# Optimization experiments

Measured on AMD Instinct MI355X. Metric: run time of the kernel, lower is better.

Reference implementation:

```python
import jax, jax.numpy as jnp
import numpy as np
import math

B, T, C, H = 4, 1024, 1024, 16
D = C // H  # head dim = 64

def setup_inputs() -> dict:
    key = jax.random.key(0)
    ks = jax.random.split(key, 10)
    s = 1.0 / math.sqrt(C)
    x = jax.random.normal(ks[0], (B, T, C), dtype=jnp.float32)
    pad = (jax.random.uniform(ks[1], (B, T)) < 0.2).astype(jnp.float32)
    # ensure first token of every row is unpadded so softmax rows are well-posed
    pad = pad.at[:, 0].set(0.0)
    Wq = jax.random.normal(ks[2], (C, C), dtype=jnp.float32) * s
    bq = jnp.zeros((C,), dtype=jnp.float32)
    Wk = jax.random.normal(ks[3], (C, C), dtype=jnp.float32) * s
    bk = jnp.zeros((C,), dtype=jnp.float32)
    Wv = jax.random.normal(ks[4], (C, C), dtype=jnp.float32) * s
    bv = jnp.zeros((C,), dtype=jnp.float32)
    Wp = jax.random.normal(ks[5], (C, C), dtype=jnp.float32) * s
    bp = jnp.zeros((C,), dtype=jnp.float32)
    return {"x": x, "x_padding_judge": pad, "Wq": Wq, "bq": bq,
            "Wk": Wk, "bk": bk, "Wv": Wv, "bv": bv, "Wp": Wp, "bp": bp}

def reference(x, x_padding_judge, Wq, bq, Wk, bk, Wv, bv, Wp, bp):
    # keep flag: 1.0 where token is real, 0.0 where padded
    keep = 1.0 - x_padding_judge                      # [B, T]
    mask = keep[:, :, None] * keep[:, None, :]        # [B, T, T] outer product
    # projections, split heads: [B, H, T, D]
    def heads(w, b):
        return (x @ w + b).reshape(B, T, H, D).transpose(0, 2, 1, 3)
    q, k, v = heads(Wq, bq), heads(Wk, bk), heads(Wv, bv)
    att = jnp.einsum('bhqd,bhkd->bhqk', q, k) * (1.0 / math.sqrt(D))
    # attn_pdrop=0 => att_full is all ones; masked_fill where mask == 0
    att = jnp.where(mask[:, None, :, :] == 0, -1e9, att)
    att = jax.nn.softmax(att, axis=-1)
    y = jnp.einsum('bhqk,bhkd->bhqd', att, v)         # [B, H, T, D]
    y = y.transpose(0, 2, 1, 3).reshape(B, T, C)
    return y @ Wp + bp
```

## Files before the change

kernel.cpp:

```cpp
#include <hip/hip_runtime.h>
#include <hip/hip_bf16.h>
#include <math.h>

#define Bb 4
#define Tt 1024
#define Cc 1024
#define Hh 16
#define Dd 64

typedef __attribute__((ext_vector_type(8))) _Float16 half8;
typedef __attribute__((ext_vector_type(4))) _Float16 half4;
typedef __attribute__((ext_vector_type(4))) float floatx4;

__device__ __forceinline__ void gl2lds16(const void* g, void* l) {
    __builtin_amdgcn_global_load_lds(
        (const __attribute__((address_space(1))) void*)g,
        (__attribute__((address_space(3))) void*)l,
        16, 0, 0);
}

__global__ __launch_bounds__(256) void convert_fp16(const float* __restrict__ s,
                                                    _Float16* __restrict__ d)
{
    const size_t i = ((size_t)blockIdx.x * 256 + threadIdx.x) * 8;
    float4 a = *(const float4*)(s + i);
    float4 b = *(const float4*)(s + i + 4);
    half8 h;
    h[0] = (_Float16)a.x; h[1] = (_Float16)a.y; h[2] = (_Float16)a.z; h[3] = (_Float16)a.w;
    h[4] = (_Float16)b.x; h[5] = (_Float16)b.y; h[6] = (_Float16)b.z; h[7] = (_Float16)b.w;
    *(half8*)(d + i) = h;
}

struct WPrep { const float* W[4]; _Float16* out[4]; };

__global__ __launch_bounds__(256) void prep_weights(WPrep p)
{
    const int z = blockIdx.z;
    const float* __restrict__ W = p.W[z];
    _Float16* __restrict__ outp = p.out[z];
    __shared__ float tile[64][65];
    const int k0  = blockIdx.y * 64;
    const int n0  = blockIdx.x * 64;
    const int tr  = threadIdx.x >> 4;
    const int tc4 = (threadIdx.x & 15) * 4;

#pragma unroll
    for (int i = 0; i < 4; ++i) {
        const int kk = tr + i * 16;
        float4 v = *(const float4*)(W + (size_t)(k0 + kk) * 1024 + n0 + tc4);
        tile[kk][tc4 + 0] = v.x;
        tile[kk][tc4 + 1] = v.y;
        tile[kk][tc4 + 2] = v.z;
        tile[kk][tc4 + 3] = v.w;
    }
    __syncthreads();
#pragma unroll
    for (int i = 0; i < 4; ++i) {
        const int n = tr + i * 16;
        half4 h;
#pragma unroll
        for (int c = 0; c < 4; ++c) h[c] = (_Float16)tile[tc4 + c][n];
        *(half4*)(outp + (size_t)(n0 + n) * 1024 + k0 + tc4) = h;
    }
}

struct QkvP { const _Float16* Wt[3]; const float* bias[3];
              _Float16* qb; _Float16* kb; _Float16* vt; };

__global__ __launch_bounds__(256) void gemm_qkv(const _Float16* __restrict__ xh, QkvP p)
{
    const int z = blockIdx.z;
    const _Float16* __restrict__ Wt   = p.Wt[z];
    const float* __restrict__    bias = p.bias[z];

    __shared__ __align__(16) _Float16 As[2][4096];
    __shared__ __align__(16) _Float16 Bs[2][4096];

    const int tid  = threadIdx.x;
    const int lane = tid & 63;
    const int w    = tid >> 6;
    const int wr   = w >> 1, wc = w & 1;
    const int quad = lane >> 4;
    const int l15  = lane & 15;
    const int bm   = blockIdx.x * 128;
    const int bn   = blockIdx.y * 128;

    const int c0 = tid, c1 = tid + 256;
    const _Float16* Ag0 = xh + (size_t)(bm + (c0 & 127)) * 1024 + (c0 >> 7) * 8;
    const _Float16* Ag1 = xh + (size_t)(bm + (c1 & 127)) * 1024 + (c1 >> 7) * 8;
    const _Float16* Bg0 = Wt + (size_t)(bn + (c0 & 127)) * 1024 + (c0 >> 7) * 8;
    const _Float16* Bg1 = Wt + (size_t)(bn + (c1 & 127)) * 1024 + (c1 >> 7) * 8;

    floatx4 acc[4][4];
#pragma unroll
    for (int i = 0; i < 4; ++i)
#pragma unroll
        for (int j = 0; j < 4; ++j)
            acc[i][j] = (floatx4){0.f, 0.f, 0.f, 0.f};

    half8 sA0 = *(const half8*)(Ag0);
    half8 sA1 = *(const half8*)(Ag1);
    half8 sB0 = *(const half8*)(Bg0);
    half8 sB1 = *(const half8*)(Bg1);
    *(half8*)&As[0][c0 * 8] = sA0;
    *(half8*)&As[0][c1 * 8] = sA1;
    *(half8*)&Bs[0][c0 * 8] = sB0;
    *(half8*)&Bs[0][c1 * 8] = sB1;
    sA0 = *(const half8*)(Ag0 + 32);
    sA1 = *(const half8*)(Ag1 + 32);
    sB0 = *(const half8*)(Bg0 + 32);
    sB1 = *(const half8*)(Bg1 + 32);
    __syncthreads();

#pragma unroll 2
    for (int kt = 0; kt < 1024; kt += 32) {
        const int cur = (kt >> 5) & 1;
        const int nxt = cur ^ 1;
        const int kf = (kt + 64 < 1024) ? kt + 64 : kt;
        half8 fA0 = *(const half8*)(Ag0 + kf);
        half8 fA1 = *(const half8*)(Ag1 + kf);
        half8 fB0 = *(const half8*)(Bg0 + kf);
        half8 fB1 = *(const half8*)(Bg1 + kf);

        half8 a[4], b[4];
#pragma unroll
        for (int i = 0; i < 4; ++i)
            a[i] = *(const half8*)&As[cur][(quad * 128 + wr * 64 + i * 16 + l15) * 8];
#pragma unroll
        for (int j = 0; j < 4; ++j)
            b[j] = *(const half8*)&Bs[cur][(quad * 128 + wc * 64 + j * 16 + l15) * 8];
#pragma unroll
        for (int i = 0; i < 4; ++i)
#pragma unroll
            for (int j = 0; j < 4; ++j)
                acc[i][j] = __builtin_amdgcn_mfma_f32_16x16x32_f16(a[i], b[j], acc[i][j], 0, 0, 0);

        *(half8*)&As[nxt][c0 * 8] = sA0;
        *(half8*)&As[nxt][c1 * 8] = sA1;
        *(half8*)&Bs[nxt][c0 * 8] = sB0;
        *(half8*)&Bs[nxt][c1 * 8] = sB1;
        __syncthreads();
        sA0 = fA0; sA1 = fA1; sB0 = fB0; sB1 = fB1;
    }

    if (z == 2) {
#pragma unroll
        for (int j = 0; j < 4; ++j) {
            const int col = bn + wc * 64 + j * 16 + l15;
            const int h = col >> 6, dd = col & 63;
            const float bj = bias[col];
#pragma unroll
            for (int i = 0; i < 4; ++i) {
                const int t0 = bm + wr * 64 + i * 16 + quad * 4;
                const int bi = t0 >> 10, t = t0 & 1023;
                half4 pk;
#pragma unroll
                for (int r = 0; r < 4; ++r) pk[r] = (_Float16)(acc[i][j][r] + bj);
                *(half4*)(p.vt + ((size_t)(bi * 16 + h) * 64 + dd) * 1024 + t) = pk;
            }
        }
    } else {
        _Float16* outp = (z == 0) ? p.qb : p.kb;
#pragma unroll
        for (int j = 0; j < 4; ++j) {
            const int col = bn + wc * 64 + j * 16 + l15;
            const int h = col >> 6, dd = col & 63;
            const float bj = bias[col];
#pragma unroll
            for (int i = 0; i < 4; ++i) {
#pragma unroll
                for (int r = 0; r < 4; ++r) {
                    const int tg = bm + wr * 64 + i * 16 + quad * 4 + r;
                    const int bi = tg >> 10, t = tg & 1023;
                    outp[((size_t)(bi * 16 + h) * 1024 + t) * 64 + dd] =
                        (_Float16)(acc[i][j][r] + bj);
                }
            }
        }
    }
}

__global__ __launch_bounds__(256) void attn_mfma(
    const _Float16* __restrict__ qb, const _Float16* __restrict__ kb,
    const _Float16* __restrict__ vt, const float* __restrict__ padj,
    _Float16* __restrict__ yh)
{
    __shared__ __align__(16) _Float16 Qs[8192];
    __shared__ __align__(16) _Float16 Ks[4096];
    __shared__ __align__(16) _Float16 Vt[4096];
    __shared__ __align__(16) _Float16 Ps[8192];
    __shared__ float keepq_s[128];
    __shared__ float keepk_s[64];

    const int tid  = threadIdx.x;
    const int lane = tid & 63;
    const int w    = tid >> 6;
    const int quad = lane >> 4;
    const int l15  = lane & 15;
    const int bh   = blockIdx.x;
    const int q0   = blockIdx.y * 128;
    const int b    = bh >> 4;
    const int h    = bh & 15;

    const _Float16* qbase = qb + (size_t)bh * Tt * Dd;
    const _Float16* kbase = kb + (size_t)bh * Tt * Dd;
    const _Float16* vbase = vt + (size_t)bh * Dd * Tt;

#pragma unroll
    for (int it = 0; it < 4; ++it) {
        const int c = it * 256 + tid;
        const int row = c & 127, kc = c >> 7;
        gl2lds16(qbase + (size_t)(q0 + row) * 64 + kc * 8, Qs + (c >> 6) * 512);
    }
    if (tid < 128) keepq_s[tid] = 1.0f - padj[b * Tt + q0 + tid];

    floatx4 O[2][4];
    floatx4 l_acc[2];
#pragma unroll
    for (int mi = 0; mi < 2; ++mi) {
#pragma unroll
        for (int dj = 0; dj < 4; ++dj) O[mi][dj] = (floatx4){0.f, 0.f, 0.f, 0.f};
        l_acc[mi] = (floatx4){0.f, 0.f, 0.f, 0.f};
    }

    half8 ones;
#pragma unroll
    for (int j = 0; j < 8; ++j) ones[j] = (_Float16)1.0f;

    constexpr float SC = 0.18033688011112042f;

    for (int kt = 0; kt < Tt; kt += 64) {
        __syncthreads();

#pragma unroll
        for (int it = 0; it < 2; ++it) {
            const int c = it * 256 + tid;
            const int key = c & 63, kc = c >> 6;
            gl2lds16(kbase + (size_t)(kt + key) * 64 + kc * 8, Ks + (c >> 6) * 512);
        }
#pragma unroll
        for (int it = 0; it < 2; ++it) {
            const int c = it * 256 + tid;
            const int dd = c & 63, kc = c >> 6;
            gl2lds16(vbase + (size_t)dd * 1024 + kt + kc * 8, Vt + (c >> 6) * 512);
        }
        if (tid < 64) keepk_s[tid] = 1.0f - padj[b * Tt + kt + tid];
        __syncthreads();

        floatx4 ST[4][2];
#pragma unroll
        for (int mk = 0; mk < 4; ++mk)
#pragma unroll
            for (int nq = 0; nq < 2; ++nq)
                ST[mk][nq] = (floatx4){0.f, 0.f, 0.f, 0.f};
#pragma unroll
        for (int ks = 0; ks < 2; ++ks) {
            half8 ak[4], bq[2];
#pragma unroll
            for (int mk = 0; mk < 4; ++mk)
                ak[mk] = *(const half8*)&Ks[((ks * 4 + quad) * 64 + mk * 16 + l15) * 8];
#pragma unroll
            for (int nq = 0; nq < 2; ++nq)
                bq[nq] = *(const half8*)&Qs[((ks * 4 + quad) * 128 + w * 32 + nq * 16 + l15) * 8];
#pragma unroll
            for (int mk = 0; mk < 4; ++mk)
#pragma unroll
                for (int nq = 0; nq < 2; ++nq)
                    ST[mk][nq] = __builtin_amdgcn_mfma_f32_16x16x32_f16(ak[mk], bq[nq], ST[mk][nq], 0, 0, 0);
        }

        const float kq0 = keepq_s[w * 32 + l15];
        const float kq1 = keepq_s[w * 32 + 16 + l15];
#pragma unroll
        for (int mk = 0; mk < 4; ++mk) {
            const float4 kk4 = *(const float4*)&keepk_s[mk * 16 + quad * 4];
            const float kkr[4] = {kk4.x, kk4.y, kk4.z, kk4.w};
#pragma unroll
            for (int nq = 0; nq < 2; ++nq) {
                const float kq = nq ? kq1 : kq0;
                half4 pk;
#pragma unroll
                for (int r = 0; r < 4; ++r) {
                    const float e = __builtin_amdgcn_exp2f(ST[mk][nq][r] * SC);
                    const float p = (kq == 0.0f) ? 1.0f : kkr[r] * e;
                    pk[r] = (_Float16)p;
                }
                *(half4*)&Ps[((mk * 2 + (quad >> 1)) * 128 + w * 32 + nq * 16 + l15) * 8 + (quad & 1) * 4] = pk;
            }
        }
        __syncthreads();

#pragma unroll
        for (int ks = 0; ks < 2; ++ks) {
            half8 ap[2], bv[4];
#pragma unroll
            for (int mi = 0; mi < 2; ++mi)
                ap[mi] = *(const half8*)&Ps[((ks * 4 + quad) * 128 + w * 32 + mi * 16 + l15) * 8];
#pragma unroll
            for (int dj = 0; dj < 4; ++dj)
                bv[dj] = *(const half8*)&Vt[((ks * 4 + quad) * 64 + dj * 16 + l15) * 8];
#pragma unroll
            for (int mi = 0; mi < 2; ++mi) {
#pragma unroll
                for (int dj = 0; dj < 4; ++dj)
                    O[mi][dj] = __builtin_amdgcn_mfma_f32_16x16x32_f16(ap[mi], bv[dj], O[mi][dj], 0, 0, 0);
                l_acc[mi] = __builtin_amdgcn_mfma_f32_16x16x32_f16(ap[mi], ones, l_acc[mi], 0, 0, 0);
            }
        }
    }

#pragma unroll
    for (int mi = 0; mi < 2; ++mi) {
#pragma unroll
        for (int r = 0; r < 4; ++r) {
            const int rowl = w * 32 + mi * 16 + quad * 4 + r;
            const int token = b * Tt + q0 + rowl;
            const float inv = 1.0f / l_acc[mi][r];
#pragma unroll
            for (int dj = 0; dj < 4; ++dj) {
                const int col = h * 64 + dj * 16 + l15;
                yh[(size_t)token * 1024 + col] = (_Float16)(O[mi][dj][r] * inv);
            }
        }
    }
}

__global__ __launch_bounds__(256) void gemm_proj(const _Float16* __restrict__ Ay,
                                                 const _Float16* __restrict__ Bt,
                                                 const float* __restrict__ bias,
                                                 float* __restrict__ out)
{
    __shared__ __align__(16) _Float16 As[2][4096];
    __shared__ __align__(16) _Float16 Bs[2][2048];

    const int tid  = threadIdx.x;
    const int lane = tid & 63;
    const int w    = tid >> 6;
    const int quad = lane >> 4;
    const int l15  = lane & 15;
    const int bm   = blockIdx.x * 128;
    const int bn   = blockIdx.y * 64;

    const int c0 = tid, c1 = tid + 256;
    const _Float16* Ag0 = Ay + (size_t)(bm + (c0 & 127)) * 1024 + (c0 >> 7) * 8;
    const _Float16* Ag1 = Ay + (size_t)(bm + (c1 & 127)) * 1024 + (c1 >> 7) * 8;
    const _Float16* Bg0 = Bt + (size_t)(bn + (c0 & 63)) * 1024 + (c0 >> 6) * 8;

    floatx4 acc[2][4];
#pragma unroll
    for (int i = 0; i < 2; ++i)
#pragma unroll
        for (int j = 0; j < 4; ++j)
            acc[i][j] = (floatx4){0.f, 0.f, 0.f, 0.f};

    half8 sA0 = *(const half8*)(Ag0);
    half8 sA1 = *(const half8*)(Ag1);
    half8 sB0 = *(const half8*)(Bg0);
    *(half8*)&As[0][c0 * 8] = sA0;
    *(half8*)&As[0][c1 * 8] = sA1;
    *(half8*)&Bs[0][c0 * 8] = sB0;
    sA0 = *(const half8*)(Ag0 + 32);
    sA1 = *(const half8*)(Ag1 + 32);
    sB0 = *(const half8*)(Bg0 + 32);
    __syncthreads();

#pragma unroll 2
    for (int kt = 0; kt < 1024; kt += 32) {
        const int cur = (kt >> 5) & 1;
        const int nxt = cur ^ 1;
        const int kf = (kt + 64 < 1024) ? kt + 64 : kt;
        half8 fA0 = *(const half8*)(Ag0 + kf);
        half8 fA1 = *(const half8*)(Ag1 + kf);
        half8 fB0 = *(const half8*)(Bg0 + kf);

        half8 a[2], b[4];
#pragma unroll
        for (int i = 0; i < 2; ++i)
            a[i] = *(const half8*)&As[cur][(quad * 128 + w * 32 + i * 16 + l15) * 8];
#pragma unroll
        for (int j = 0; j < 4; ++j)
            b[j] = *(const half8*)&Bs[cur][(quad * 64 + j * 16 + l15) * 8];
#pragma unroll
        for (int i = 0; i < 2; ++i)
#pragma unroll
            for (int j = 0; j < 4; ++j)
                acc[i][j] = __builtin_amdgcn_mfma_f32_16x16x32_f16(a[i], b[j], acc[i][j], 0, 0, 0);

        *(half8*)&As[nxt][c0 * 8] = sA0;
        *(half8*)&As[nxt][c1 * 8] = sA1;
        *(half8*)&Bs[nxt][c0 * 8] = sB0;
        __syncthreads();
        sA0 = fA0; sA1 = fA1; sB0 = fB0;
    }

#pragma unroll
    for (int j = 0; j < 4; ++j) {
        const int col = bn + j * 16 + l15;
        const float bj = bias[col];
#pragma unroll
        for (int i = 0; i < 2; ++i) {
            const int row = bm + w * 32 + i * 16 + quad * 4;
            float* o = out + (size_t)row * 1024 + col;
#pragma unroll
            for (int r = 0; r < 4; ++r)
                o[(size_t)r * 1024] = acc[i][j][r] + bj;
        }
    }
}

extern "C" void kernel_launch(void* const* d_in, const int* in_sizes, int n_in,
                              void* d_out, int out_size, void* d_ws, size_t ws_size,
                              hipStream_t stream)
{
    const float* x    = (const float*)d_in[0];
    const float* padj = (const float*)d_in[1];
    const float* Wq   = (const float*)d_in[2];
    const float* bq   = (const float*)d_in[3];
    const float* Wk   = (const float*)d_in[4];
    const float* bk   = (const float*)d_in[5];
    const float* Wv   = (const float*)d_in[6];
    const float* bv   = (const float*)d_in[7];
    const float* Wp   = (const float*)d_in[8];
    const float* bp   = (const float*)d_in[9];
    float* out = (float*)d_out;

    const size_t MB = 1024 * 1024;
    char* ws = (char*)d_ws;
    _Float16* xh  = (_Float16*)(ws);
    _Float16* Wt0 = (_Float16*)(ws +  8 * MB);
    _Float16* Wt1 = (_Float16*)(ws + 10 * MB);
    _Float16* Wt2 = (_Float16*)(ws + 12 * MB);
    _Float16* Wtp = (_Float16*)(ws + 14 * MB);
    _Float16* qb  = (_Float16*)(ws + 16 * MB);
    _Float16* kb  = (_Float16*)(ws + 24 * MB);
    _Float16* vtb = (_Float16*)(ws + 32 * MB);
    _Float16* yh  = (_Float16*)(ws + 40 * MB);

    convert_fp16<<<2048, 256, 0, stream>>>(x, xh);

    WPrep wp;
    wp.W[0] = Wq; wp.W[1] = Wk; wp.W[2] = Wv; wp.W[3] = Wp;
    wp.out[0] = Wt0; wp.out[1] = Wt1; wp.out[2] = Wt2; wp.out[3] = Wtp;
    prep_weights<<<dim3(16, 16, 4), 256, 0, stream>>>(wp);

    QkvP qp;
    qp.Wt[0] = Wt0; qp.Wt[1] = Wt1; qp.Wt[2] = Wt2;
    qp.bias[0] = bq; qp.bias[1] = bk; qp.bias[2] = bv;
    qp.qb = qb; qp.kb = kb; qp.vt = vtb;
    gemm_qkv<<<dim3(32, 8, 3), 256, 0, stream>>>(xh, qp);

    attn_mfma<<<dim3(64, 8), 256, 0, stream>>>(qb, kb, vtb, padj, yh);

    gemm_proj<<<dim3(32, 16), 256, 0, stream>>>(yh, Wtp, bp, out);
}
```

Baseline: 213.6 us.

## Pre-swizzle operands into MFMA fragment layout and drop LDS staging in GEMMs

The fp16 copies of x, the weights and the attention output are now written in a tiled layout in which each 16-row by 32-k MFMA fragment is a contiguous 1 KB block. This lets the QKV and projection GEMMs load operand fragments straight from global memory into registers with no LDS staging and no __syncthreads. The cost is that operand reuse across waves now relies on L2/L1 caching instead of shared memory, so global traffic per block goes up. The reworked convert kernel also launches 256 blocks, each converting a 16-row strip.

```diff
diff --git a/kernel.cpp b/kernel.cpp
--- a/kernel.cpp
+++ b/kernel.cpp
@@ -12,6 +12,7 @@
 typedef __attribute__((ext_vector_type(4))) _Float16 half4;
 typedef __attribute__((ext_vector_type(4))) float floatx4;
 
+
 __device__ __forceinline__ void gl2lds16(const void* g, void* l) {
     __builtin_amdgcn_global_load_lds(
         (const __attribute__((address_space(1))) void*)g,
@@ -22,13 +23,21 @@
 __global__ __launch_bounds__(256) void convert_fp16(const float* __restrict__ s,
                                                     _Float16* __restrict__ d)
 {
-    const size_t i = ((size_t)blockIdx.x * 256 + threadIdx.x) * 8;
-    float4 a = *(const float4*)(s + i);
-    float4 b = *(const float4*)(s + i + 4);
-    half8 h;
-    h[0] = (_Float16)a.x; h[1] = (_Float16)a.y; h[2] = (_Float16)a.z; h[3] = (_Float16)a.w;
-    h[4] = (_Float16)b.x; h[5] = (_Float16)b.y; h[6] = (_Float16)b.z; h[7] = (_Float16)b.w;
-    *(half8*)(d + i) = h;
+    const int m16 = blockIdx.x;
+    const int r   = threadIdx.x & 15;
+    const int kc0 = threadIdx.x >> 4;
+    const float* src = s + (size_t)(m16 * 16 + r) * 1024;
+    _Float16*   dst = d + (size_t)m16 * 16384 + r * 8;
+#pragma unroll
+    for (int c8 = 0; c8 < 8; ++c8) {
+        const int kc = kc0 + c8 * 16;
+        float4 a = *(const float4*)(src + kc * 8);
+        float4 b = *(const float4*)(src + kc * 8 + 4);
+        half8 h;
+        h[0] = (_Float16)a.x; h[1] = (_Float16)a.y; h[2] = (_Float16)a.z; h[3] = (_Float16)a.w;
+        h[4] = (_Float16)b.x; h[5] = (_Float16)b.y; h[6] = (_Float16)b.z; h[7] = (_Float16)b.w;
+        *(half8*)(dst + kc * 128) = h;
+    }
 }
 
 struct WPrep { const float* W[4]; _Float16* out[4]; };
@@ -56,11 +65,12 @@
     __syncthreads();
 #pragma unroll
     for (int i = 0; i < 4; ++i) {
-        const int n = tr + i * 16;
         half4 h;
 #pragma unroll
-        for (int c = 0; c < 4; ++c) h[c] = (_Float16)tile[tc4 + c][n];
-        *(half4*)(outp + (size_t)(n0 + n) * 1024 + k0 + tc4) = h;
+        for (int c = 0; c < 4; ++c) h[c] = (_Float16)tile[tc4 + c][tr + i * 16];
+        _Float16* dst = outp + (size_t)((n0 >> 4) + i) * 16384
+                        + ((k0 + tc4) >> 3) * 128 + tr * 8 + (tc4 & 7);
+        *(half4*)dst = h;
     }
 }
 
@@ -72,9 +82,6 @@
     const int z = blockIdx.z;
     const _Float16* __restrict__ Wt   = p.Wt[z];
     const float* __restrict__    bias = p.bias[z];
-
-    __shared__ __align__(16) _Float16 As[2][4096];
-    __shared__ __align__(16) _Float16 Bs[2][4096];
 
     const int tid  = threadIdx.x;
     const int lane = tid & 63;
@@ -85,11 +92,14 @@
     const int bm   = blockIdx.x * 128;
     const int bn   = blockIdx.y * 128;
 
-    const int c0 = tid, c1 = tid + 256;
-    const _Float16* Ag0 = xh + (size_t)(bm + (c0 & 127)) * 1024 + (c0 >> 7) * 8;
-    const _Float16* Ag1 = xh + (size_t)(bm + (c1 & 127)) * 1024 + (c1 >> 7) * 8;
-    const _Float16* Bg0 = Wt + (size_t)(bn + (c0 & 127)) * 1024 + (c0 >> 7) * 8;
-    const _Float16* Bg1 = Wt + (size_t)(bn + (c1 & 127)) * 1024 + (c1 >> 7) * 8;
+    const _Float16* Ap[4];
+    const _Float16* Bp[4];
+#pragma unroll
+    for (int i = 0; i < 4; ++i)
+        Ap[i] = xh + (size_t)((bm >> 4) + wr * 4 + i) * 16384 + lane * 8;
+#pragma unroll
+    for (int j = 0; j < 4; ++j)
+        Bp[j] = Wt + (size_t)((bn >> 4) + wc * 4 + j) * 16384 + lane * 8;
 
     floatx4 acc[4][4];
 #pragma unroll
@@ -98,49 +108,35 @@
         for (int j = 0; j < 4; ++j)
             acc[i][j] = (floatx4){0.f, 0.f, 0.f, 0.f};
 
-    half8 sA0 = *(const half8*)(Ag0);
-    half8 sA1 = *(const half8*)(Ag1);
-    half8 sB0 = *(const half8*)(Bg0);
-    half8 sB1 = *(const half8*)(Bg1);
-    *(half8*)&As[0][c0 * 8] = sA0;
-    *(half8*)&As[0][c1 * 8] = sA1;
-    *(half8*)&Bs[0][c0 * 8] = sB0;
-    *(half8*)&Bs[0][c1 * 8] = sB1;
-    sA0 = *(const half8*)(Ag0 + 32);
-    sA1 = *(const half8*)(Ag1 + 32);
-    sB0 = *(const half8*)(Bg0 + 32);
-    sB1 = *(const half8*)(Bg1 + 32);
-    __syncthreads();
-
-#pragma unroll 2
-    for (int kt = 0; kt < 1024; kt += 32) {
-        const int cur = (kt >> 5) & 1;
-        const int nxt = cur ^ 1;
-        const int kf = (kt + 64 < 1024) ? kt + 64 : kt;
-        half8 fA0 = *(const half8*)(Ag0 + kf);
-        half8 fA1 = *(const half8*)(Ag1 + kf);
-        half8 fB0 = *(const half8*)(Bg0 + kf);
-        half8 fB1 = *(const half8*)(Bg1 + kf);
-
-        half8 a[4], b[4];
+    half8 a0[4], b0[4];
+#pragma unroll
+    for (int i = 0; i < 4; ++i) a0[i] = *(const half8*)(Ap[i]);
+#pragma unroll
+    for (int j = 0; j < 4; ++j) b0[j] = *(const half8*)(Bp[j]);
+
+    for (int kt = 0; kt < 1024; kt += 64) {
+        half8 a1[4], b1[4];
+        const size_t o1 = (size_t)(kt + 32) * 16;
+#pragma unroll
+        for (int i = 0; i < 4; ++i) a1[i] = *(const half8*)(Ap[i] + o1);
+#pragma unroll
+        for (int j = 0; j < 4; ++j) b1[j] = *(const half8*)(Bp[j] + o1);
 #pragma unroll
         for (int i = 0; i < 4; ++i)
-            a[i] = *(const half8*)&As[cur][(quad * 128 + wr * 64 + i * 16 + l15) * 8];
-#pragma unroll
-        for (int j = 0; j < 4; ++j)
-            b[j] = *(const half8*)&Bs[cur][(quad * 128 + wc * 64 + j * 16 + l15) * 8];
+#pragma unroll
+            for (int j = 0; j < 4; ++j)
+                acc[i][j] = __builtin_amdgcn_mfma_f32_16x16x32_f16(a0[i], b0[j], acc[i][j], 0, 0, 0);
+
+        const size_t o2 = (kt + 64 < 1024) ? (size_t)(kt + 64) * 16 : 0;
+#pragma unroll
+        for (int i = 0; i < 4; ++i) a0[i] = *(const half8*)(Ap[i] + o2);
+#pragma unroll
+        for (int j = 0; j < 4; ++j) b0[j] = *(const half8*)(Bp[j] + o2);
 #pragma unroll
         for (int i = 0; i < 4; ++i)
 #pragma unroll
             for (int j = 0; j < 4; ++j)
-                acc[i][j] = __builtin_amdgcn_mfma_f32_16x16x32_f16(a[i], b[j], acc[i][j], 0, 0, 0);
-
-        *(half8*)&As[nxt][c0 * 8] = sA0;
-        *(half8*)&As[nxt][c1 * 8] = sA1;
-        *(half8*)&Bs[nxt][c0 * 8] = sB0;
-        *(half8*)&Bs[nxt][c1 * 8] = sB1;
-        __syncthreads();
-        sA0 = fA0; sA1 = fA1; sB0 = fB0; sB1 = fB1;
+                acc[i][j] = __builtin_amdgcn_mfma_f32_16x16x32_f16(a1[i], b1[j], acc[i][j], 0, 0, 0);
     }
 
     if (z == 2) {
@@ -313,13 +309,14 @@
     for (int mi = 0; mi < 2; ++mi) {
 #pragma unroll
         for (int r = 0; r < 4; ++r) {
-            const int rowl = w * 32 + mi * 16 + quad * 4 + r;
+            const int rowl  = w * 32 + mi * 16 + quad * 4 + r;
             const int token = b * Tt + q0 + rowl;
             const float inv = 1.0f / l_acc[mi][r];
+            const size_t tb = (size_t)(token >> 4) * 16384 + (token & 15) * 8;
 #pragma unroll
             for (int dj = 0; dj < 4; ++dj) {
                 const int col = h * 64 + dj * 16 + l15;
-                yh[(size_t)token * 1024 + col] = (_Float16)(O[mi][dj][r] * inv);
+                yh[tb + (col >> 3) * 128 + (col & 7)] = (_Float16)(O[mi][dj][r] * inv);
             }
         }
     }
@@ -330,9 +327,6 @@
                                                  const float* __restrict__ bias,
                                                  float* __restrict__ out)
 {
-    __shared__ __align__(16) _Float16 As[2][4096];
-    __shared__ __align__(16) _Float16 Bs[2][2048];
-
     const int tid  = threadIdx.x;
     const int lane = tid & 63;
     const int w    = tid >> 6;
@@ -341,10 +335,14 @@
     const int bm   = blockIdx.x * 128;
     const int bn   = blockIdx.y * 64;
 
-    const int c0 = tid, c1 = tid + 256;
-    const _Float16* Ag0 = Ay + (size_t)(bm + (c0 & 127)) * 1024 + (c0 >> 7) * 8;
-    const _Float16* Ag1 = Ay + (size_t)(bm + (c1 & 127)) * 1024 + (c1 >> 7) * 8;
-    const _Float16* Bg0 = Bt + (size_t)(bn + (c0 & 63)) * 1024 + (c0 >> 6) * 8;
+    const _Float16* Ap[2];
+    const _Float16* Bp[4];
+#pragma unroll
+    for (int i = 0; i < 2; ++i)
+        Ap[i] = Ay + (size_t)((bm >> 4) + w * 2 + i) * 16384 + lane * 8;
+#pragma unroll
+    for (int j = 0; j < 4; ++j)
+        Bp[j] = Bt + (size_t)((bn >> 4) + j) * 16384 + lane * 8;
 
     floatx4 acc[2][4];
 #pragma unroll
@@ -353,44 +351,35 @@
         for (int j = 0; j < 4; ++j)
             acc[i][j] = (floatx4){0.f, 0.f, 0.f, 0.f};
 
-    half8 sA0 = *(const half8*)(Ag0);
-    half8 sA1 = *(const half8*)(Ag1);
-    half8 sB0 = *(const half8*)(Bg0);
-    *(half8*)&As[0][c0 * 8] = sA0;
-    *(half8*)&As[0][c1 * 8] = sA1;
-    *(half8*)&Bs[0][c0 * 8] = sB0;
-    sA0 = *(const half8*)(Ag0 + 32);
-    sA1 = *(const half8*)(Ag1 + 32);
-    sB0 = *(const half8*)(Bg0 + 32);
-    __syncthreads();
-
-#pragma unroll 2
-    for (int kt = 0; kt < 1024; kt += 32) {
-        const int cur = (kt >> 5) & 1;
-        const int nxt = cur ^ 1;
-        const int kf = (kt + 64 < 1024) ? kt + 64 : kt;
-        half8 fA0 = *(const half8*)(Ag0 + kf);
-        half8 fA1 = *(const half8*)(Ag1 + kf);
-        half8 fB0 = *(const half8*)(Bg0 + kf);
-
-        half8 a[2], b[4];
+    half8 a0[2], b0[4];
+#pragma unroll
+    for (int i = 0; i < 2; ++i) a0[i] = *(const half8*)(Ap[i]);
+#pragma unroll
+    for (int j = 0; j < 4; ++j) b0[j] = *(const half8*)(Bp[j]);
+
+    for (int kt = 0; kt < 1024; kt += 64) {
+        half8 a1[2], b1[4];
+        const size_t o1 = (size_t)(kt + 32) * 16;
+#pragma unroll
+        for (int i = 0; i < 2; ++i) a1[i] = *(const half8*)(Ap[i] + o1);
+#pragma unroll
+        for (int j = 0; j < 4; ++j) b1[j] = *(const half8*)(Bp[j] + o1);
 #pragma unroll
         for (int i = 0; i < 2; ++i)
-            a[i] = *(const half8*)&As[cur][(quad * 128 + w * 32 + i * 16 + l15) * 8];
-#pragma unroll
-        for (int j = 0; j < 4; ++j)
-            b[j] = *(const half8*)&Bs[cur][(quad * 64 + j * 16 + l15) * 8];
+#pragma unroll
+            for (int j = 0; j < 4; ++j)
+                acc[i][j] = __builtin_amdgcn_mfma_f32_16x16x32_f16(a0[i], b0[j], acc[i][j], 0, 0, 0);
+
+        const size_t o2 = (kt + 64 < 1024) ? (size_t)(kt + 64) * 16 : 0;
+#pragma unroll
+        for (int i = 0; i < 2; ++i) a0[i] = *(const half8*)(Ap[i] + o2);
+#pragma unroll
+        for (int j = 0; j < 4; ++j) b0[j] = *(const half8*)(Bp[j] + o2);
 #pragma unroll
         for (int i = 0; i < 2; ++i)
 #pragma unroll
             for (int j = 0; j < 4; ++j)
-                acc[i][j] = __builtin_amdgcn_mfma_f32_16x16x32_f16(a[i], b[j], acc[i][j], 0, 0, 0);
-
-        *(half8*)&As[nxt][c0 * 8] = sA0;
-        *(half8*)&As[nxt][c1 * 8] = sA1;
-        *(half8*)&Bs[nxt][c0 * 8] = sB0;
-        __syncthreads();
-        sA0 = fA0; sA1 = fA1; sB0 = fB0;
+                acc[i][j] = __builtin_amdgcn_mfma_f32_16x16x32_f16(a1[i], b1[j], acc[i][j], 0, 0, 0);
     }
 
 #pragma unroll
@@ -436,7 +425,7 @@
     _Float16* vtb = (_Float16*)(ws + 32 * MB);
     _Float16* yh  = (_Float16*)(ws + 40 * MB);
 
-    convert_fp16<<<2048, 256, 0, stream>>>(x, xh);
+    convert_fp16<<<256, 256, 0, stream>>>(x, xh);
 
     WPrep wp;
     wp.W[0] = Wq; wp.W[1] = Wk; wp.W[2] = Wv; wp.W[3] = Wp;
```

Measured after the change: 189.0 us. 11.5% less time.
